# Performance work log

Measured on AMD Instinct MI355X. Metric: run time of the kernel, lower is better.

The kernel has to match this reference:

```python
import jax, jax.numpy as jnp
import numpy as np

K = 2  # kernel_size = stride = 2 along each of the 4 spatial dims


def _windows(a, k):
    # a: [B, C, D1, D2, D3, D4] -> [B, C, D1/k, D2/k, D3/k, D4/k, k**4]
    B, C, D1, D2, D3, D4 = a.shape
    a = a.reshape(B, C, D1 // k, k, D2 // k, k, D3 // k, k, D4 // k, k)
    a = a.transpose(0, 1, 2, 4, 6, 8, 3, 5, 7, 9)
    return a.reshape(B, C, D1 // k, D2 // k, D3 // k, D4 // k, k ** 4)


def setup_inputs() -> dict:
    key = jax.random.key(0)
    input = jax.random.normal(key, (8, 2, 32, 16, 16, 16, 16), dtype=jnp.float32)
    return {"input": input}


def reference(input):
    # input: [B, 2, C, D1, D2, D3, D4]; dim 1 = (real, imag)
    r = input[:, 0]  # [B, C, D1, D2, D3, D4]
    i = input[:, 1]
    mod = jnp.sqrt(r * r + i * i)  # complex modulus

    mod_w = _windows(mod, K)  # [B, C, O1, O2, O3, O4, K^4]
    r_w = _windows(r, K)
    i_w = _windows(i, K)

    # argmax of modulus within each 2x2x2x2 window (= return_indices of max_pool4d)
    idx = jnp.argmax(mod_w, axis=-1)[..., None]  # [B, C, O1, O2, O3, O4, 1]

    # dual gather: pick real/imag values at the max-modulus location
    r_out = jnp.take_along_axis(r_w, idx, axis=-1)[..., 0]
    i_out = jnp.take_along_axis(i_w, idx, axis=-1)[..., 0]
    return jnp.stack((r_out, i_out), axis=1)  # [B, 2, C, O1, O2, O3, O4]
```

## Files before the change

### kernel.cpp

```cpp
#include <hip/hip_runtime.h>
#include <math.h>


__global__ __launch_bounds__(256) void cmaxpool4d_kernel(
    const float* __restrict__ in, float* __restrict__ out)
{
#pragma clang fp contract(off)
    const int t = blockIdx.x * blockDim.x + threadIdx.x;

    const int t4 = t & 3;
    const int o3 = (t >> 2) & 7;
    const int o2 = (t >> 5) & 7;
    const int o1 = (t >> 8) & 7;
    const int c  = (t >> 11) & 31;
    const int b  = t >> 16;

    const size_t planeElems = 65536;
    const float* __restrict__ pr = in + (((size_t)b * 2 + 0) * 32 + c) * planeElems;
    const float* __restrict__ pi = in + (((size_t)b * 2 + 1) * 32 + c) * planeElems;

    float bm0 = -1.0f, br0 = 0.0f, bi0 = 0.0f;
    float bm1 = -1.0f, br1 = 0.0f, bi1 = 0.0f;

    const int d4b = 4 * t4;

#pragma unroll
    for (int k1 = 0; k1 < 2; ++k1) {
        const int d1 = 2 * o1 + k1;
#pragma unroll
        for (int k2 = 0; k2 < 2; ++k2) {
            const int d2 = 2 * o2 + k2;
#pragma unroll
            for (int k3 = 0; k3 < 2; ++k3) {
                const int d3 = 2 * o3 + k3;
                const size_t off = (((size_t)d1 * 16 + d2) * 16 + d3) * 16 + d4b;
                const float4 r4 = *reinterpret_cast<const float4*>(pr + off);
                const float4 i4 = *reinterpret_cast<const float4*>(pi + off);

                float rr, ii, s, m;
                rr = r4.x * r4.x; ii = i4.x * i4.x; s = rr + ii; m = __fsqrt_rn(s);
                if (m > bm0) { bm0 = m; br0 = r4.x; bi0 = i4.x; }
                rr = r4.y * r4.y; ii = i4.y * i4.y; s = rr + ii; m = __fsqrt_rn(s);
                if (m > bm0) { bm0 = m; br0 = r4.y; bi0 = i4.y; }
                rr = r4.z * r4.z; ii = i4.z * i4.z; s = rr + ii; m = __fsqrt_rn(s);
                if (m > bm1) { bm1 = m; br1 = r4.z; bi1 = i4.z; }
                rr = r4.w * r4.w; ii = i4.w * i4.w; s = rr + ii; m = __fsqrt_rn(s);
                if (m > bm1) { bm1 = m; br1 = r4.w; bi1 = i4.w; }
            }
        }
    }

    const size_t outPlane = 4096;
    const size_t oOff = (size_t)o1 * 512 + (size_t)o2 * 64 + (size_t)o3 * 8 + 2 * t4;
    float* __restrict__ qr = out + (((size_t)b * 2 + 0) * 32 + c) * outPlane + oOff;
    float* __restrict__ qi = out + (((size_t)b * 2 + 1) * 32 + c) * outPlane + oOff;

    *reinterpret_cast<float2*>(qr) = make_float2(br0, br1);
    *reinterpret_cast<float2*>(qi) = make_float2(bi0, bi1);
}

extern "C" void kernel_launch(void* const* d_in, const int* in_sizes, int n_in,
                              void* d_out, int out_size, void* d_ws, size_t ws_size,
                              hipStream_t stream) {
    (void)in_sizes; (void)n_in; (void)d_ws; (void)ws_size; (void)out_size;
    const float* in = (const float*)d_in[0];
    float* out = (float*)d_out;

    const int nThreads = 8 * 32 * 8 * 8 * 8 * 4;
    const int block = 256;
    const int grid = nThreads / block;
    cmaxpool4d_kernel<<<grid, block, 0, stream>>>(in, out);
}
```

Before: 27.71 us.

## Remap threads so each wavefront reads contiguous d3/d4 rows and merges windows via shuffles

```diff
diff --git a/kernel.cpp b/kernel.cpp
--- a/kernel.cpp
+++ b/kernel.cpp
@@ -2,61 +2,85 @@
 #include <math.h>
 
 
-__global__ __launch_bounds__(256) void cmaxpool4d_kernel(
+__global__ __launch_bounds__(256) void cmaxpool4d_v2(
     const float* __restrict__ in, float* __restrict__ out)
 {
 #pragma clang fp contract(off)
-    const int t = blockIdx.x * blockDim.x + threadIdx.x;
+    const int tid = blockIdx.x * 256 + threadIdx.x;
+    const int W = tid >> 6;
+    const int L = threadIdx.x & 63;
 
-    const int t4 = t & 3;
-    const int o3 = (t >> 2) & 7;
-    const int o2 = (t >> 5) & 7;
-    const int o1 = (t >> 8) & 7;
-    const int c  = (t >> 11) & 31;
-    const int b  = t >> 16;
+    const int o2p = W & 3;
+    const int o1  = (W >> 2) & 7;
+    const int c   = (W >> 5) & 31;
+    const int b   = W >> 10;
 
-    const size_t planeElems = 65536;
-    const float* __restrict__ pr = in + (((size_t)b * 2 + 0) * 32 + c) * planeElems;
-    const float* __restrict__ pi = in + (((size_t)b * 2 + 1) * 32 + c) * planeElems;
+    const int qd4 = L & 3;
+    const int d3  = L >> 2;
+    const int k3  = d3 & 1;
+    const int o3  = L >> 3;
 
-    float bm0 = -1.0f, br0 = 0.0f, bi0 = 0.0f;
-    float bm1 = -1.0f, br1 = 0.0f, bi1 = 0.0f;
+    const size_t plane = 65536;
+    const float* __restrict__ pr = in + (((size_t)b * 2 + 0) * 32 + c) * plane;
+    const float* __restrict__ pi = in + (((size_t)b * 2 + 1) * 32 + c) * plane;
+    const int laneOff = 4 * L;
 
-    const int d4b = 4 * t4;
+    for (int jo2 = 0; jo2 < 2; ++jo2) {
+        const int o2 = 2 * o2p + jo2;
+
+        float bm0 = -1.0f, br0 = 0.0f, bi0 = 0.0f;
+        float bm1 = -1.0f, br1 = 0.0f, bi1 = 0.0f;
+        int bw0 = 0, bw1 = 0;
 
 #pragma unroll
-    for (int k1 = 0; k1 < 2; ++k1) {
-        const int d1 = 2 * o1 + k1;
+        for (int k1 = 0; k1 < 2; ++k1) {
+            const int d1 = 2 * o1 + k1;
 #pragma unroll
-        for (int k2 = 0; k2 < 2; ++k2) {
-            const int d2 = 2 * o2 + k2;
-#pragma unroll
-            for (int k3 = 0; k3 < 2; ++k3) {
-                const int d3 = 2 * o3 + k3;
-                const size_t off = (((size_t)d1 * 16 + d2) * 16 + d3) * 16 + d4b;
+            for (int k2 = 0; k2 < 2; ++k2) {
+                const int d2 = 2 * o2 + k2;
+                const size_t off = (size_t)(d1 * 16 + d2) * 256 + laneOff;
                 const float4 r4 = *reinterpret_cast<const float4*>(pr + off);
                 const float4 i4 = *reinterpret_cast<const float4*>(pi + off);
+                const int wb = k1 * 8 + k2 * 4 + k3 * 2;
 
                 float rr, ii, s, m;
                 rr = r4.x * r4.x; ii = i4.x * i4.x; s = rr + ii; m = __fsqrt_rn(s);
-                if (m > bm0) { bm0 = m; br0 = r4.x; bi0 = i4.x; }
+                if (m > bm0) { bm0 = m; br0 = r4.x; bi0 = i4.x; bw0 = wb; }
                 rr = r4.y * r4.y; ii = i4.y * i4.y; s = rr + ii; m = __fsqrt_rn(s);
-                if (m > bm0) { bm0 = m; br0 = r4.y; bi0 = i4.y; }
+                if (m > bm0) { bm0 = m; br0 = r4.y; bi0 = i4.y; bw0 = wb + 1; }
                 rr = r4.z * r4.z; ii = i4.z * i4.z; s = rr + ii; m = __fsqrt_rn(s);
-                if (m > bm1) { bm1 = m; br1 = r4.z; bi1 = i4.z; }
+                if (m > bm1) { bm1 = m; br1 = r4.z; bi1 = i4.z; bw1 = wb; }
                 rr = r4.w * r4.w; ii = i4.w * i4.w; s = rr + ii; m = __fsqrt_rn(s);
-                if (m > bm1) { bm1 = m; br1 = r4.w; bi1 = i4.w; }
+                if (m > bm1) { bm1 = m; br1 = r4.w; bi1 = i4.w; bw1 = wb + 1; }
             }
         }
+
+        {
+            const float mo = __shfl_xor(bm0, 4);
+            const int   wo = __shfl_xor(bw0, 4);
+            const float ro = __shfl_xor(br0, 4);
+            const float io = __shfl_xor(bi0, 4);
+            if (mo > bm0 || (mo == bm0 && wo < bw0)) {
+                bm0 = mo; br0 = ro; bi0 = io; bw0 = wo;
+            }
+        }
+        {
+            const float mo = __shfl_xor(bm1, 4);
+            const int   wo = __shfl_xor(bw1, 4);
+            const float ro = __shfl_xor(br1, 4);
+            const float io = __shfl_xor(bi1, 4);
+            if (mo > bm1 || (mo == bm1 && wo < bw1)) {
+                bm1 = mo; br1 = ro; bi1 = io; bw1 = wo;
+            }
+        }
+
+        const int ch = k3;
+        float* __restrict__ q = out + (((size_t)b * 2 + ch) * 32 + c) * 4096
+                              + (size_t)o1 * 512 + (size_t)o2 * 64
+                              + (size_t)o3 * 8 + 2 * qd4;
+        const float2 v = ch ? make_float2(bi0, bi1) : make_float2(br0, br1);
+        *reinterpret_cast<float2*>(q) = v;
     }
-
-    const size_t outPlane = 4096;
-    const size_t oOff = (size_t)o1 * 512 + (size_t)o2 * 64 + (size_t)o3 * 8 + 2 * t4;
-    float* __restrict__ qr = out + (((size_t)b * 2 + 0) * 32 + c) * outPlane + oOff;
-    float* __restrict__ qi = out + (((size_t)b * 2 + 1) * 32 + c) * outPlane + oOff;
-
-    *reinterpret_cast<float2*>(qr) = make_float2(br0, br1);
-    *reinterpret_cast<float2*>(qi) = make_float2(bi0, bi1);
 }
 
 extern "C" void kernel_launch(void* const* d_in, const int* in_sizes, int n_in,
@@ -66,8 +90,8 @@
     const float* in = (const float*)d_in[0];
     float* out = (float*)d_out;
 
-    const int nThreads = 8 * 32 * 8 * 8 * 8 * 4;
+    const int nThreads = 8192 * 64;
     const int block = 256;
     const int grid = nThreads / block;
-    cmaxpool4d_kernel<<<grid, block, 0, stream>>>(in, out);
+    cmaxpool4d_v2<<<grid, block, 0, stream>>>(in, out);
 }
```

New measurement: 27.35 us. No clear change (-1.3%).
